# Kernel tuning notes

Hardware: AMD Instinct MI355X
Metric: run time of the kernel (lower is better)

## Reference

```python
import jax, jax.numpy as jnp
import numpy as np

B, C, H, W = 8, 16, 1024, 1024
ALPHA = 0.2  # contamination weight per neighbor


def setup_inputs() -> dict:
    key = jax.random.key(0)
    x = jax.random.normal(key, (B, C, H, W), dtype=jnp.float32)
    return {"x": x}


def reference(x):
    # Original module: for every grid cell (src), add 0.2*x[src] to each of its
    # 8 in-bounds neighbors in y (y initialized to x, x never mutated).
    # Scatter-to-neighbors == gather-from-neighbors: y = x + 0.2 * sum of 8 neighbors.
    xp = jnp.pad(x, ((0, 0), (0, 0), (1, 1), (1, 1)))  # zero pad -> out-of-bounds skipped
    nb = (
        xp[:, :, 0:-2, 1:-1] + xp[:, :, 2:, 1:-1] +      # up, down
        xp[:, :, 1:-1, 0:-2] + xp[:, :, 1:-1, 2:] +      # left, right
        xp[:, :, 0:-2, 0:-2] + xp[:, :, 0:-2, 2:] +      # diagonals
        xp[:, :, 2:, 0:-2] + xp[:, :, 2:, 2:]
    )
    return x + ALPHA * nb
```

## Files before the change

### kernel.cpp

```cpp
#include <hip/hip_runtime.h>
#include <hip/hip_bf16.h>


#define ALPHA 0.2f
#define ROWS 16

typedef float f4 __attribute__((ext_vector_type(4)));

__device__ __forceinline__ void load6(const float* __restrict__ p, int w, int W,
                                      float v[6]) {
    const f4 c = *reinterpret_cast<const f4*>(p + w);
    v[0] = (w > 0) ? p[w - 1] : 0.0f;
    v[1] = c.x; v[2] = c.y; v[3] = c.z; v[4] = c.w;
    v[5] = (w + 4 < W) ? p[w + 4] : 0.0f;
}

__global__ __launch_bounds__(256)
void contamination_kernel(const float* __restrict__ x, float* __restrict__ y,
                          int H, int W) {
    const int tilesPerImg = H / ROWS;
    const int tile = blockIdx.x;
    const int img  = tile / tilesPerImg;
    const int h0   = (tile - img * tilesPerImg) * ROWS;
    const size_t base = ((size_t)img * H + (size_t)h0) * W;
    const int w = threadIdx.x * 4;

    const float* __restrict__ row = x + base;
    float* __restrict__ orow = y + base;

    float t[6], m[6], b[6];
#pragma unroll
    for (int j = 0; j < 6; ++j) t[j] = 0.0f;

    if (h0 > 0) load6(row - W, w, W, t);
    load6(row, w, W, m);

#pragma unroll
    for (int i = 0; i < ROWS; ++i) {
        if (h0 + i + 1 < H) {
            load6(row + W, w, W, b);
        } else {
#pragma unroll
            for (int j = 0; j < 6; ++j) b[j] = 0.0f;
        }

        f4 o;
#pragma unroll
        for (int j = 0; j < 4; ++j) {
            const float nb = t[j] + t[j + 1] + t[j + 2] +
                             b[j] + b[j + 1] + b[j + 2] +
                             m[j] + m[j + 2];
            o[j] = m[j + 1] + ALPHA * nb;
        }
        __builtin_nontemporal_store(o, reinterpret_cast<f4*>(orow + w));

#pragma unroll
        for (int j = 0; j < 6; ++j) { t[j] = m[j]; m[j] = b[j]; }
        row += W; orow += W;
    }
}

extern "C" void kernel_launch(void* const* d_in, const int* in_sizes, int n_in,
                              void* d_out, int out_size, void* d_ws, size_t ws_size,
                              hipStream_t stream) {
    const float* x = (const float*)d_in[0];
    float* y = (float*)d_out;

    const int W = 1024;
    const int H = 1024;
    const int n = in_sizes[0];
    const int blocks = n / (W * ROWS);

    contamination_kernel<<<dim3(blocks), dim3(W / 4), 0, stream>>>(x, y, H, W);
}
```

Before: 203.7 us.

## Use wave shuffles for halo, prefetch next row, cache row sums, swizzle blocks

Each thread now gets its left and right neighbour values from adjacent lanes with shuffles, so only wave-edge lanes issue scalar halo loads. Horizontal 3-sums are computed once per row and reused for the rows above and below. The next row is prefetched one iteration ahead, and rows per block double to cut vertical halo re-reads. Blocks are remapped so consecutive block IDs are spread across the XCD-interleaved tile space, and dimensions become compile-time constants. The costs are fewer blocks in flight and extra cross-lane shuffle work.

```diff
diff --git a/kernel.cpp b/kernel.cpp
--- a/kernel.cpp
+++ b/kernel.cpp
@@ -3,59 +3,88 @@
 
 
 #define ALPHA 0.2f
-#define ROWS 16
+#define ROWS 32
+#define W 1024
+#define H 1024
 
 typedef float f4 __attribute__((ext_vector_type(4)));
 
-__device__ __forceinline__ void load6(const float* __restrict__ p, int w, int W,
-                                      float v[6]) {
-    const f4 c = *reinterpret_cast<const f4*>(p + w);
-    v[0] = (w > 0) ? p[w - 1] : 0.0f;
-    v[1] = c.x; v[2] = c.y; v[3] = c.z; v[4] = c.w;
-    v[5] = (w + 4 < W) ? p[w + 4] : 0.0f;
+struct Pend { f4 c; float eL, eR; };
+
+__device__ __forceinline__ void loadrow(const float* __restrict__ p, int w,
+                                        int lane, Pend& P) {
+    P.c = *reinterpret_cast<const f4*>(p + w);
+    P.eL = 0.0f; P.eR = 0.0f;
+    if (lane == 0 && w > 0)       P.eL = p[w - 1];
+    if (lane == 63 && w + 4 < W)  P.eR = p[w + 4];
+}
+
+__device__ __forceinline__ void convert(const Pend& P, int lane, f4& s, f4& c) {
+    const float l = __shfl_up(P.c.w, 1);
+    const float r = __shfl_down(P.c.x, 1);
+    const float eL = (lane == 0)  ? P.eL : l;
+    const float eR = (lane == 63) ? P.eR : r;
+    c = P.c;
+    s.x = eL    + P.c.x + P.c.y;
+    s.y = P.c.x + P.c.y + P.c.z;
+    s.z = P.c.y + P.c.z + P.c.w;
+    s.w = P.c.z + P.c.w + eR;
 }
 
 __global__ __launch_bounds__(256)
-void contamination_kernel(const float* __restrict__ x, float* __restrict__ y,
-                          int H, int W) {
+void contamination_kernel(const float* __restrict__ x, float* __restrict__ y) {
     const int tilesPerImg = H / ROWS;
-    const int tile = blockIdx.x;
+    const int cpx = gridDim.x >> 3;
+    const int bid = blockIdx.x;
+    const int tile = (bid & 7) * cpx + (bid >> 3);
+
     const int img  = tile / tilesPerImg;
-    const int h0   = (tile - img * tilesPerImg) * ROWS;
-    const size_t base = ((size_t)img * H + (size_t)h0) * W;
-    const int w = threadIdx.x * 4;
+    const int trow = tile - img * tilesPerImg;
+    const int h0   = trow * ROWS;
+    const size_t base = ((size_t)img * H + (size_t)h0) * (size_t)W;
 
-    const float* __restrict__ row = x + base;
-    float* __restrict__ orow = y + base;
+    const int tid  = threadIdx.x;
+    const int lane = tid & 63;
+    const int w    = tid * 4;
 
-    float t[6], m[6], b[6];
-#pragma unroll
-    for (int j = 0; j < 6; ++j) t[j] = 0.0f;
+    const float* __restrict__ row  = x + base;
+    float* __restrict__       orow = y + base;
 
-    if (h0 > 0) load6(row - W, w, W, t);
-    load6(row, w, W, m);
+    f4 t_s, m_s, m_c;
+    if (h0 > 0) {
+        Pend P; loadrow(row - W, w, lane, P);
+        f4 dc; convert(P, lane, t_s, dc);
+    } else {
+        t_s.x = t_s.y = t_s.z = t_s.w = 0.0f;
+    }
+
+    { Pend P; loadrow(row, w, lane, P); convert(P, lane, m_s, m_c); }
+
+    Pend pend;
+    loadrow(row + W, w, lane, pend);
 
 #pragma unroll
     for (int i = 0; i < ROWS; ++i) {
+        f4 b_s, b_c;
         if (h0 + i + 1 < H) {
-            load6(row + W, w, W, b);
+            convert(pend, lane, b_s, b_c);
         } else {
-#pragma unroll
-            for (int j = 0; j < 6; ++j) b[j] = 0.0f;
+            b_s.x = b_s.y = b_s.z = b_s.w = 0.0f;
+            b_c = b_s;
         }
+
+        if (i < ROWS - 1 && h0 + i + 2 < H)
+            loadrow(row + 2 * W, w, lane, pend);
 
         f4 o;
 #pragma unroll
         for (int j = 0; j < 4; ++j) {
-            const float nb = t[j] + t[j + 1] + t[j + 2] +
-                             b[j] + b[j + 1] + b[j + 2] +
-                             m[j] + m[j + 2];
-            o[j] = m[j + 1] + ALPHA * nb;
+            const float nb = t_s[j] + b_s[j] + m_s[j] - m_c[j];
+            o[j] = fmaf(ALPHA, nb, m_c[j]);
         }
         __builtin_nontemporal_store(o, reinterpret_cast<f4*>(orow + w));
 
-#pragma unroll
-        for (int j = 0; j < 6; ++j) { t[j] = m[j]; m[j] = b[j]; }
+        t_s = m_s; m_s = b_s; m_c = b_c;
         row += W; orow += W;
     }
 }
@@ -66,10 +95,8 @@
     const float* x = (const float*)d_in[0];
     float* y = (float*)d_out;
 
-    const int W = 1024;
-    const int H = 1024;
     const int n = in_sizes[0];
-    const int blocks = n / (W * ROWS);
+    const int blocks = (n / W) / ROWS;
 
-    contamination_kernel<<<dim3(blocks), dim3(W / 4), 0, stream>>>(x, y, H, W);
+    contamination_kernel<<<dim3(blocks), dim3(W / 4), 0, stream>>>(x, y);
 }
```

New measurement: 218.2 us. +7.1%, slower.
